# Optimization experiments

Hardware: AMD Instinct MI355X
Metric: run time of the kernel (lower is better)

## Reference

```python
import jax, jax.numpy as jnp
import numpy as np

EMBED_DIM = 1024
NUM_HEADS = 16
HEAD_DIM = EMBED_DIM // NUM_HEADS
B, T = 2, 2048


def setup_inputs() -> dict:
    key = jax.random.key(0)
    ks = jax.random.split(key, 9)
    s = 1.0 / np.sqrt(EMBED_DIM)
    return {
        "x": jax.random.normal(ks[0], (B, T, EMBED_DIM), dtype=jnp.float32),
        "W_q": jax.random.uniform(ks[1], (EMBED_DIM, EMBED_DIM), jnp.float32, -s, s),
        "b_q": jax.random.uniform(ks[2], (EMBED_DIM,), jnp.float32, -s, s),
        "W_k": jax.random.uniform(ks[3], (EMBED_DIM, EMBED_DIM), jnp.float32, -s, s),
        "b_k": jax.random.uniform(ks[4], (EMBED_DIM,), jnp.float32, -s, s),
        "W_v": jax.random.uniform(ks[5], (EMBED_DIM, EMBED_DIM), jnp.float32, -s, s),
        "b_v": jax.random.uniform(ks[6], (EMBED_DIM,), jnp.float32, -s, s),
        "W_o": jax.random.uniform(ks[7], (EMBED_DIM, EMBED_DIM), jnp.float32, -s, s),
        "b_o": jax.random.uniform(ks[8], (EMBED_DIM,), jnp.float32, -s, s),
    }


def reference(x, W_q, b_q, W_k, b_k, W_v, b_v, W_o, b_o):
    Bv, Tv, C = x.shape
    # QKV projections (torch Linear: x @ W.T + b); split into heads -> (B,H,T,Dh)
    def proj(W, b):
        return (x @ W.T + b).reshape(Bv, Tv, NUM_HEADS, HEAD_DIM).transpose(0, 2, 1, 3)
    q, k, v = proj(W_q, b_q), proj(W_k, b_k), proj(W_v, b_v)
    scale = 1.0 / np.sqrt(HEAD_DIM).astype(np.float32)
    scores = jnp.einsum("bhqd,bhkd->bhqk", q, k) * scale  # (B,H,T,T)
    causal = jnp.tril(jnp.ones((Tv, Tv), dtype=bool))
    scores = jnp.where(causal, scores, -jnp.inf)
    attn = jax.nn.softmax(scores, axis=-1)
    # dropout is identity in eval / p=0
    out = jnp.einsum("bhqk,bhkd->bhqd", attn, v)  # (B,H,T,Dh)
    out = out.transpose(0, 2, 1, 3).reshape(Bv, Tv, C)
    return out @ W_o.T + b_o
```

## Files before the change

kernel.cpp:

```cpp
#include <hip/hip_runtime.h>
#include <hip/hip_bf16.h>


typedef __bf16 bf16;
typedef __attribute__((ext_vector_type(8))) __bf16 bf16x8;
typedef __attribute__((ext_vector_type(4))) __bf16 bf16x4;
typedef __attribute__((ext_vector_type(4))) float floatx4;
typedef __attribute__((ext_vector_type(4))) short short4v;

#define LOG2E 1.44269504088896340736f

__device__ __forceinline__ void gl2lds16(const void* g, void* l) {
  __builtin_amdgcn_global_load_lds((const __attribute__((address_space(1))) void*)g,
                                   (__attribute__((address_space(3))) void*)l, 16, 0, 0);
}

__device__ __forceinline__ floatx4 mfma16(bf16x4 a, bf16x4 b, floatx4 c) {
#if __has_builtin(__builtin_amdgcn_mfma_f32_16x16x16_bf16)
  return __builtin_amdgcn_mfma_f32_16x16x16_bf16(a, b, c, 0, 0, 0);
#elif __has_builtin(__builtin_amdgcn_mfma_f32_16x16x16bf16_1k)
  return __builtin_amdgcn_mfma_f32_16x16x16bf16_1k(
      __builtin_bit_cast(short4v, a), __builtin_bit_cast(short4v, b), c, 0, 0, 0);
#else
  floatx4 d = c;
  asm volatile("v_mfma_f32_16x16x16_bf16 %0, %1, %2, %0"
               : "+v"(d) : "v"(a), "v"(b));
  return d;
#endif
}

__global__ __launch_bounds__(256) void cast_all(
    const float* __restrict__ x, const float* __restrict__ wq,
    const float* __restrict__ wk, const float* __restrict__ wv,
    const float* __restrict__ wo, bf16* __restrict__ dst)
{
  const size_t M1 = (size_t)1 << 20;
  size_t i4 = ((size_t)blockIdx.x * 256 + threadIdx.x) * 4;
  const float* src = x;
  size_t off = i4;
  if (i4 >= 4 * M1) {
    size_t r = i4 - 4 * M1;
    int seg = (int)(r >> 20);
    off = r & (M1 - 1);
    src = (seg == 0) ? wq : (seg == 1) ? wk : (seg == 2) ? wv : wo;
  }
  float4 f = *(const float4*)(src + off);
  bf16x4 o = { (bf16)f.x, (bf16)f.y, (bf16)f.z, (bf16)f.w };
  *(bf16x4*)(dst + i4) = o;
}

template<bool F32OUT, bool QKV, int BN>
__global__ __launch_bounds__(256, 3) void gemm_bt(
    const bf16* __restrict__ A, const bf16* __restrict__ Wb,
    const float* __restrict__ bq, const float* __restrict__ bk,
    const float* __restrict__ bv, void* __restrict__ outb,
    bf16* __restrict__ vt, int M, int N, int K, float qscale)
{
  __shared__ bf16 As[128 * 64];
  __shared__ bf16 Bs[BN * 64];
  const int tid = threadIdx.x;
  const int lane = tid & 63;
  const int wid = tid >> 6;
  const int l15 = lane & 15, l4 = lane >> 4;
  constexpr int I = (BN == 128) ? 4 : 2;
  const int wr = (BN == 128) ? (wid >> 1) : wid;
  const int wc = (BN == 128) ? (wid & 1) : 0;

  const bf16* W;
  const float* bias;
  float osc = 1.0f;
  int n0, mat = 0;
  bf16* outh;
  float* outf;
  if (QKV) {
    mat = blockIdx.x >> 3;
    n0 = (blockIdx.x & 7) << 7;
    W = Wb + ((size_t)mat << 20);
    bias = (mat == 0) ? bq : (mat == 1 ? bk : bv);
    if (mat == 0) osc = qscale;
    outh = (bf16*)outb + ((size_t)mat << 22);
    outf = nullptr;
  } else {
    n0 = blockIdx.x * BN;
    W = Wb;
    bias = bq;
    outf = (float*)outb;
    outh = nullptr;
  }
  const int m0 = blockIdx.y << 7;

  floatx4 acc[I][4] = {};

  for (int k0 = 0; k0 < K; k0 += 64) {
#pragma unroll
    for (int it = 0; it < 4; ++it) {
      int c = it * 256 + tid;
      int row = c >> 3, gs = ((c & 7) ^ (row & 7)) << 3;
      gl2lds16(A + (size_t)(m0 + row) * K + k0 + gs, As + c * 8);
    }
#pragma unroll
    for (int it = 0; it < BN / 32; ++it) {
      int c = it * 256 + tid;
      int row = c >> 3, gs = ((c & 7) ^ (row & 7)) << 3;
      gl2lds16(W + (size_t)(n0 + row) * K + k0 + gs, Bs + c * 8);
    }
    __syncthreads();
#pragma unroll
    for (int kk = 0; kk < 2; ++kk) {
      bf16x8 af[I], bfr[4];
#pragma unroll
      for (int i = 0; i < I; ++i) {
        int r = wr * (I * 16) + i * 16 + l15;
        int g = (kk * 4 + l4) ^ (r & 7);
        af[i] = *(const bf16x8*)(As + r * 64 + g * 8);
      }
#pragma unroll
      for (int j = 0; j < 4; ++j) {
        int r = wc * 64 + j * 16 + l15;
        int g = (kk * 4 + l4) ^ (r & 7);
        bfr[j] = *(const bf16x8*)(Bs + r * 64 + g * 8);
      }
#pragma unroll
      for (int i = 0; i < I; ++i)
#pragma unroll
        for (int j = 0; j < 4; ++j)
          acc[i][j] = __builtin_amdgcn_mfma_f32_16x16x32_bf16(af[i], bfr[j], acc[i][j], 0, 0, 0);
    }
    __syncthreads();
  }

  if (QKV && mat == 2) {
#pragma unroll
    for (int j = 0; j < 4; ++j) {
      int col = n0 + wc * 64 + j * 16 + l15;
      float bv_ = bias[col];
      int h = col >> 6, d = col & 63;
#pragma unroll
      for (int i = 0; i < I; ++i) {
        int row = m0 + wr * (I * 16) + i * 16 + l4 * 4;
        int bb = row >> 11, t = row & 2047;
        int tp = (t & ~31) | (((t >> 2) & 3) << 3) | (((t >> 4) & 1) << 2);
        bf16x4 pk;
#pragma unroll
        for (int rg = 0; rg < 4; ++rg) pk[rg] = (bf16)(acc[i][j][rg] + bv_);
        *(bf16x4*)(vt + (((size_t)(bb * 16 + h)) << 17) + ((size_t)d << 11) + tp) = pk;
      }
    }
    return;
  }

#pragma unroll
  for (int j = 0; j < 4; ++j) {
    int col = n0 + wc * 64 + j * 16 + l15;
    float bv_ = bias[col];
#pragma unroll
    for (int i = 0; i < I; ++i) {
#pragma unroll
      for (int rg = 0; rg < 4; ++rg) {
        int row = m0 + wr * (I * 16) + i * 16 + l4 * 4 + rg;
        float v = (acc[i][j][rg] + bv_) * osc;
        if (F32OUT) outf[(size_t)row * N + col] = v;
        else        outh[(size_t)row * N + col] = (bf16)v;
      }
    }
  }
}

__global__ __launch_bounds__(256, 4) void attn_kernel(
    const bf16* __restrict__ Q, const bf16* __restrict__ Kg,
    const bf16* __restrict__ Vt, bf16* __restrict__ AO)
{
  constexpr int T = 2048, C = 1024;
  __shared__ bf16 Ks[2][64 * 64];
  __shared__ bf16 Vts[2][64 * 64];

  const int tid = threadIdx.x;
  const int lane = tid & 63;
  const int w = tid >> 6;
  const int l15 = lane & 15, l4 = lane >> 4;

  const int u = blockIdx.x;
  const int bh = u & 31;
  const int qt = 31 - (u >> 5);
  const int q0 = qt << 6;
  const int nkt = qt + 1;
  const size_t base = ((size_t)(bh >> 4) * T) * C + (bh & 15) * 64;
  const bf16* vtb = Vt + ((size_t)bh << 17);

  auto stageK = [&](int j0, int bufi) {
#pragma unroll
    for (int it = 0; it < 2; ++it) {
      int c = it * 256 + tid;
      int row = c >> 3, g = (c & 7) ^ (row & 7);
      gl2lds16(Kg + base + (size_t)(j0 + row) * C + g * 8, &Ks[bufi][c * 8]);
    }
  };
  auto stageV = [&](int j0, int bufi) {
#pragma unroll
    for (int it = 0; it < 2; ++it) {
      int c = it * 256 + tid;
      int d = c >> 3, g = (c & 7) ^ (d & 7);
      gl2lds16(vtb + ((size_t)d << 11) + j0 + g * 8, &Vts[bufi][c * 8]);
    }
  };

  const int q = q0 + w * 16 + l15;

  bf16x8 qf[2];
  {
    const bf16* qp = Q + base + (size_t)q * C + l4 * 8;
    qf[0] = *(const bf16x8*)(qp);
    qf[1] = *(const bf16x8*)(qp + 32);
  }

  floatx4 o[4] = {};
  float mrow = -1e38f, lrow = 0.f;

  stageK(0, 0);
  stageV(0, 0);

  for (int jt = 0; jt < nkt; ++jt) {
    __syncthreads();
    const int cur = jt & 1;
    if (jt + 1 < nkt) {
      stageK((jt + 1) << 6, cur ^ 1);
      stageV((jt + 1) << 6, cur ^ 1);
    }
    const int j0 = jt << 6;

    floatx4 s4[4] = {};
#pragma unroll
    for (int kk = 0; kk < 2; ++kk) {
#pragma unroll
      for (int tj = 0; tj < 4; ++tj) {
        int r = tj * 16 + l15;
        int g = (kk * 4 + l4) ^ (r & 7);
        bf16x8 kf = *(const bf16x8*)(&Ks[cur][r * 64 + g * 8]);
        s4[tj] = __builtin_amdgcn_mfma_f32_16x16x32_bf16(kf, qf[kk], s4[tj], 0, 0, 0);
      }
    }

    if (jt == nkt - 1) {
#pragma unroll
      for (int tj = 0; tj < 4; ++tj) {
        int j = j0 + tj * 16 + l4 * 4;
#pragma unroll
        for (int rg = 0; rg < 4; ++rg)
          if (j + rg > q) s4[tj][rg] = -3e38f;
      }
    }

    float mx = -3e38f;
#pragma unroll
    for (int tj = 0; tj < 4; ++tj)
#pragma unroll
      for (int rg = 0; rg < 4; ++rg)
        mx = fmaxf(mx, s4[tj][rg]);
    mx = fmaxf(mx, __shfl_xor(mx, 16, 64));
    mx = fmaxf(mx, __shfl_xor(mx, 32, 64));
    float mnew = fmaxf(mrow, mx);
    float al = __builtin_amdgcn_exp2f(mrow - mnew);
    mrow = mnew;
    float ps = 0.f;
#pragma unroll
    for (int tj = 0; tj < 4; ++tj)
#pragma unroll
      for (int rg = 0; rg < 4; ++rg) {
        float e = __builtin_amdgcn_exp2f(s4[tj][rg] - mnew);
        s4[tj][rg] = e;
        ps += e;
      }
    ps += __shfl_xor(ps, 16, 64);
    ps += __shfl_xor(ps, 32, 64);
    lrow = lrow * al + ps;

    if (!__all(al == 1.f)) {
#pragma unroll
      for (int td = 0; td < 4; ++td)
#pragma unroll
        for (int rg = 0; rg < 4; ++rg)
          o[td][rg] *= al;
    }

    bf16x4 pf[4];
#pragma unroll
    for (int tj = 0; tj < 4; ++tj) {
      bf16x4 pk = { (bf16)s4[tj][0], (bf16)s4[tj][1],
                    (bf16)s4[tj][2], (bf16)s4[tj][3] };
      pf[tj] = pk;
    }

#pragma unroll
    for (int tk = 0; tk < 2; ++tk) {
#pragma unroll
      for (int td = 0; td < 4; ++td) {
        int r = td * 16 + l15;
        int g = (tk * 4 + l4) ^ (r & 7);
        bf16x8 vf = *(const bf16x8*)(&Vts[cur][r * 64 + g * 8]);
        bf16x4 lo = { vf[0], vf[1], vf[2], vf[3] };
        bf16x4 hi = { vf[4], vf[5], vf[6], vf[7] };
        o[td] = mfma16(lo, pf[tk * 2], o[td]);
        o[td] = mfma16(hi, pf[tk * 2 + 1], o[td]);
      }
    }
  }

  float inv = 1.0f / lrow;
#pragma unroll
  for (int td = 0; td < 4; ++td) {
    bf16x4 ok = { (bf16)(o[td][0] * inv), (bf16)(o[td][1] * inv),
                  (bf16)(o[td][2] * inv), (bf16)(o[td][3] * inv) };
    *(bf16x4*)(AO + base + (size_t)q * C + td * 16 + l4 * 4) = ok;
  }
}

extern "C" void kernel_launch(void* const* d_in, const int* in_sizes, int n_in,
                              void* d_out, int out_size, void* d_ws, size_t ws_size,
                              hipStream_t stream) {
  const float* x  = (const float*)d_in[0];
  const float* Wq = (const float*)d_in[1];
  const float* bq = (const float*)d_in[2];
  const float* Wk = (const float*)d_in[3];
  const float* bk = (const float*)d_in[4];
  const float* Wv = (const float*)d_in[5];
  const float* bv = (const float*)d_in[6];
  const float* Wo = (const float*)d_in[7];
  const float* bo = (const float*)d_in[8];

  bf16* ws = (bf16*)d_ws;
  const size_t M1 = (size_t)1 << 20;
  bf16* xb  = ws;
  bf16* wqb = ws + 4 * M1;
  bf16* wob = ws + 7 * M1;
  bf16* Qp  = ws + 8 * M1;
  bf16* Vtp = ws + 16 * M1;
  bf16* AOp = ws + 20 * M1;

  cast_all<<<8192, 256, 0, stream>>>(x, Wq, Wk, Wv, Wo, ws);
  gemm_bt<false, true, 128><<<dim3(24, 32), 256, 0, stream>>>(
      xb, wqb, bq, bk, bv, (void*)Qp, Vtp, 4096, 1024, 1024, 0.125f * LOG2E);
  attn_kernel<<<1024, 256, 0, stream>>>(Qp, Qp + 4 * M1, Vtp, AOp);
  gemm_bt<true, false, 64><<<dim3(16, 32), 256, 0, stream>>>(
      AOp, wob, bo, nullptr, nullptr, d_out, nullptr, 4096, 1024, 1024, 1.0f);
}
```

Measured before the change: 174.5 us.

## Fuse x cast into QKV GEMM and pair causal query tiles per attention block

Stops converting x to bf16 in a separate pass. The QKV GEMM now loads fp32 x tiles straight into LDS and converts them to bf16 when building MFMA fragments, which doubles the A-tile LDS footprint and adds conversion work inside the GEMM inner loop. Each attention block now handles two query tiles (qt and 31-qt), so every block does the same amount of causal work. The grid is halved, and K/V prefetch carries over between the two segments.

```diff
diff --git a/kernel.cpp b/kernel.cpp
--- a/kernel.cpp
+++ b/kernel.cpp
@@ -29,21 +29,16 @@
 #endif
 }
 
-__global__ __launch_bounds__(256) void cast_all(
-    const float* __restrict__ x, const float* __restrict__ wq,
-    const float* __restrict__ wk, const float* __restrict__ wv,
-    const float* __restrict__ wo, bf16* __restrict__ dst)
+__global__ __launch_bounds__(256) void cast_w(
+    const float* __restrict__ wq, const float* __restrict__ wk,
+    const float* __restrict__ wv, const float* __restrict__ wo,
+    bf16* __restrict__ dst)
 {
   const size_t M1 = (size_t)1 << 20;
   size_t i4 = ((size_t)blockIdx.x * 256 + threadIdx.x) * 4;
-  const float* src = x;
-  size_t off = i4;
-  if (i4 >= 4 * M1) {
-    size_t r = i4 - 4 * M1;
-    int seg = (int)(r >> 20);
-    off = r & (M1 - 1);
-    src = (seg == 0) ? wq : (seg == 1) ? wk : (seg == 2) ? wv : wo;
-  }
+  int seg = (int)(i4 >> 20);
+  size_t off = i4 & (M1 - 1);
+  const float* src = (seg == 0) ? wq : (seg == 1) ? wk : (seg == 2) ? wv : wo;
   float4 f = *(const float4*)(src + off);
   bf16x4 o = { (bf16)f.x, (bf16)f.y, (bf16)f.z, (bf16)f.w };
   *(bf16x4*)(dst + i4) = o;
@@ -51,12 +46,12 @@
 
 template<bool F32OUT, bool QKV, int BN>
 __global__ __launch_bounds__(256, 3) void gemm_bt(
-    const bf16* __restrict__ A, const bf16* __restrict__ Wb,
+    const void* __restrict__ Aany, const bf16* __restrict__ Wb,
     const float* __restrict__ bq, const float* __restrict__ bk,
     const float* __restrict__ bv, void* __restrict__ outb,
     bf16* __restrict__ vt, int M, int N, int K, float qscale)
 {
-  __shared__ bf16 As[128 * 64];
+  __shared__ char smemA[QKV ? 128 * 64 * 4 : 128 * 64 * 2];
   __shared__ bf16 Bs[BN * 64];
   const int tid = threadIdx.x;
   const int lane = tid & 63;
@@ -92,11 +87,25 @@
   floatx4 acc[I][4] = {};
 
   for (int k0 = 0; k0 < K; k0 += 64) {
-#pragma unroll
-    for (int it = 0; it < 4; ++it) {
-      int c = it * 256 + tid;
-      int row = c >> 3, gs = ((c & 7) ^ (row & 7)) << 3;
-      gl2lds16(A + (size_t)(m0 + row) * K + k0 + gs, As + c * 8);
+    if (QKV) {
+      const float* Af = (const float*)Aany;
+      float* Asf = (float*)smemA;
+#pragma unroll
+      for (int it = 0; it < 8; ++it) {
+        int c = it * 256 + tid;
+        int row = c >> 4, g = c & 15;
+        int gs = (g & 8) | ((g & 7) ^ (row & 7));
+        gl2lds16(Af + (size_t)(m0 + row) * K + k0 + gs * 4, Asf + c * 4);
+      }
+    } else {
+      const bf16* Ah = (const bf16*)Aany;
+      bf16* Ash = (bf16*)smemA;
+#pragma unroll
+      for (int it = 0; it < 4; ++it) {
+        int c = it * 256 + tid;
+        int row = c >> 3, gs = ((c & 7) ^ (row & 7)) << 3;
+        gl2lds16(Ah + (size_t)(m0 + row) * K + k0 + gs, Ash + c * 8);
+      }
     }
 #pragma unroll
     for (int it = 0; it < BN / 32; ++it) {
@@ -111,8 +120,21 @@
 #pragma unroll
       for (int i = 0; i < I; ++i) {
         int r = wr * (I * 16) + i * 16 + l15;
-        int g = (kk * 4 + l4) ^ (r & 7);
-        af[i] = *(const bf16x8*)(As + r * 64 + g * 8);
+        if (QKV) {
+          const float* Asf = (const float*)smemA;
+          int m2 = kk * 8 + l4 * 2;
+          int s1 = (m2 & 8) | ((m2 & 7) ^ (r & 7));
+          int s2 = ((m2 + 1) & 8) | (((m2 + 1) & 7) ^ (r & 7));
+          floatx4 fa = *(const floatx4*)(Asf + r * 64 + s1 * 4);
+          floatx4 fb = *(const floatx4*)(Asf + r * 64 + s2 * 4);
+          bf16x8 v = { (bf16)fa[0], (bf16)fa[1], (bf16)fa[2], (bf16)fa[3],
+                       (bf16)fb[0], (bf16)fb[1], (bf16)fb[2], (bf16)fb[3] };
+          af[i] = v;
+        } else {
+          const bf16* Ash = (const bf16*)smemA;
+          int g = (kk * 4 + l4) ^ (r & 7);
+          af[i] = *(const bf16x8*)(Ash + r * 64 + g * 8);
+        }
       }
 #pragma unroll
       for (int j = 0; j < 4; ++j) {
@@ -181,9 +203,7 @@
 
   const int u = blockIdx.x;
   const int bh = u & 31;
-  const int qt = 31 - (u >> 5);
-  const int q0 = qt << 6;
-  const int nkt = qt + 1;
+  const int p = u >> 5;
   const size_t base = ((size_t)(bh >> 4) * T) * C + (bh & 15) * 64;
   const bf16* vtb = Vt + ((size_t)bh << 17);
 
@@ -204,113 +224,122 @@
     }
   };
 
-  const int q = q0 + w * 16 + l15;
-
-  bf16x8 qf[2];
-  {
-    const bf16* qp = Q + base + (size_t)q * C + l4 * 8;
-    qf[0] = *(const bf16x8*)(qp);
-    qf[1] = *(const bf16x8*)(qp + 32);
-  }
-
-  floatx4 o[4] = {};
-  float mrow = -1e38f, lrow = 0.f;
-
+  const int qts[2] = { 31 - p, p };
+  int g = 0;
   stageK(0, 0);
   stageV(0, 0);
 
-  for (int jt = 0; jt < nkt; ++jt) {
-    __syncthreads();
-    const int cur = jt & 1;
-    if (jt + 1 < nkt) {
-      stageK((jt + 1) << 6, cur ^ 1);
-      stageV((jt + 1) << 6, cur ^ 1);
-    }
-    const int j0 = jt << 6;
-
-    floatx4 s4[4] = {};
-#pragma unroll
-    for (int kk = 0; kk < 2; ++kk) {
+  for (int seg = 0; seg < 2; ++seg) {
+    const int qt = qts[seg];
+    const int q0 = qt << 6;
+    const int nkt = qt + 1;
+    const int q = q0 + w * 16 + l15;
+
+    bf16x8 qf[2];
+    {
+      const bf16* qp = Q + base + (size_t)q * C + l4 * 8;
+      qf[0] = *(const bf16x8*)(qp);
+      qf[1] = *(const bf16x8*)(qp + 32);
+    }
+    floatx4 o[4] = {};
+    float mrow = -1e38f, lrow = 0.f;
+
+    for (int jt = 0; jt < nkt; ++jt, ++g) {
+      __syncthreads();
+      const int cur = g & 1;
+      if (jt + 1 < nkt) {
+        stageK((jt + 1) << 6, cur ^ 1);
+        stageV((jt + 1) << 6, cur ^ 1);
+      } else if (seg == 0) {
+        stageK(0, cur ^ 1);
+        stageV(0, cur ^ 1);
+      }
+      const int j0 = jt << 6;
+
+      floatx4 s4[4] = {};
+#pragma unroll
+      for (int kk = 0; kk < 2; ++kk) {
+#pragma unroll
+        for (int tj = 0; tj < 4; ++tj) {
+          int r = tj * 16 + l15;
+          int gg = (kk * 4 + l4) ^ (r & 7);
+          bf16x8 kf = *(const bf16x8*)(&Ks[cur][r * 64 + gg * 8]);
+          s4[tj] = __builtin_amdgcn_mfma_f32_16x16x32_bf16(kf, qf[kk], s4[tj], 0, 0, 0);
+        }
+      }
+
+      if (jt == nkt - 1) {
+#pragma unroll
+        for (int tj = 0; tj < 4; ++tj) {
+          int j = j0 + tj * 16 + l4 * 4;
+#pragma unroll
+          for (int rg = 0; rg < 4; ++rg)
+            if (j + rg > q) s4[tj][rg] = -3e38f;
+        }
+      }
+
+      float mx = -3e38f;
+#pragma unroll
+      for (int tj = 0; tj < 4; ++tj)
+#pragma unroll
+        for (int rg = 0; rg < 4; ++rg)
+          mx = fmaxf(mx, s4[tj][rg]);
+      mx = fmaxf(mx, __shfl_xor(mx, 16, 64));
+      mx = fmaxf(mx, __shfl_xor(mx, 32, 64));
+      float mnew = fmaxf(mrow, mx);
+      float al = __builtin_amdgcn_exp2f(mrow - mnew);
+      mrow = mnew;
+      float ps = 0.f;
+#pragma unroll
+      for (int tj = 0; tj < 4; ++tj)
+#pragma unroll
+        for (int rg = 0; rg < 4; ++rg) {
+          float e = __builtin_amdgcn_exp2f(s4[tj][rg] - mnew);
+          s4[tj][rg] = e;
+          ps += e;
+        }
+      ps += __shfl_xor(ps, 16, 64);
+      ps += __shfl_xor(ps, 32, 64);
+      lrow = lrow * al + ps;
+
+      if (!__all(al == 1.f)) {
+#pragma unroll
+        for (int td = 0; td < 4; ++td)
+#pragma unroll
+          for (int rg = 0; rg < 4; ++rg)
+            o[td][rg] *= al;
+      }
+
+      bf16x4 pf[4];
 #pragma unroll
       for (int tj = 0; tj < 4; ++tj) {
-        int r = tj * 16 + l15;
-        int g = (kk * 4 + l4) ^ (r & 7);
-        bf16x8 kf = *(const bf16x8*)(&Ks[cur][r * 64 + g * 8]);
-        s4[tj] = __builtin_amdgcn_mfma_f32_16x16x32_bf16(kf, qf[kk], s4[tj], 0, 0, 0);
-      }
-    }
-
-    if (jt == nkt - 1) {
-#pragma unroll
-      for (int tj = 0; tj < 4; ++tj) {
-        int j = j0 + tj * 16 + l4 * 4;
-#pragma unroll
-        for (int rg = 0; rg < 4; ++rg)
-          if (j + rg > q) s4[tj][rg] = -3e38f;
-      }
-    }
-
-    float mx = -3e38f;
-#pragma unroll
-    for (int tj = 0; tj < 4; ++tj)
-#pragma unroll
-      for (int rg = 0; rg < 4; ++rg)
-        mx = fmaxf(mx, s4[tj][rg]);
-    mx = fmaxf(mx, __shfl_xor(mx, 16, 64));
-    mx = fmaxf(mx, __shfl_xor(mx, 32, 64));
-    float mnew = fmaxf(mrow, mx);
-    float al = __builtin_amdgcn_exp2f(mrow - mnew);
-    mrow = mnew;
-    float ps = 0.f;
-#pragma unroll
-    for (int tj = 0; tj < 4; ++tj)
-#pragma unroll
-      for (int rg = 0; rg < 4; ++rg) {
-        float e = __builtin_amdgcn_exp2f(s4[tj][rg] - mnew);
-        s4[tj][rg] = e;
-        ps += e;
-      }
-    ps += __shfl_xor(ps, 16, 64);
-    ps += __shfl_xor(ps, 32, 64);
-    lrow = lrow * al + ps;
-
-    if (!__all(al == 1.f)) {
-#pragma unroll
-      for (int td = 0; td < 4; ++td)
-#pragma unroll
-        for (int rg = 0; rg < 4; ++rg)
-          o[td][rg] *= al;
-    }
-
-    bf16x4 pf[4];
-#pragma unroll
-    for (int tj = 0; tj < 4; ++tj) {
-      bf16x4 pk = { (bf16)s4[tj][0], (bf16)s4[tj][1],
-                    (bf16)s4[tj][2], (bf16)s4[tj][3] };
-      pf[tj] = pk;
-    }
-
-#pragma unroll
-    for (int tk = 0; tk < 2; ++tk) {
-#pragma unroll
-      for (int td = 0; td < 4; ++td) {
-        int r = td * 16 + l15;
-        int g = (tk * 4 + l4) ^ (r & 7);
-        bf16x8 vf = *(const bf16x8*)(&Vts[cur][r * 64 + g * 8]);
-        bf16x4 lo = { vf[0], vf[1], vf[2], vf[3] };
-        bf16x4 hi = { vf[4], vf[5], vf[6], vf[7] };
-        o[td] = mfma16(lo, pf[tk * 2], o[td]);
-        o[td] = mfma16(hi, pf[tk * 2 + 1], o[td]);
-      }
-    }
-  }
-
-  float inv = 1.0f / lrow;
-#pragma unroll
-  for (int td = 0; td < 4; ++td) {
-    bf16x4 ok = { (bf16)(o[td][0] * inv), (bf16)(o[td][1] * inv),
-                  (bf16)(o[td][2] * inv), (bf16)(o[td][3] * inv) };
-    *(bf16x4*)(AO + base + (size_t)q * C + td * 16 + l4 * 4) = ok;
+        bf16x4 pk = { (bf16)s4[tj][0], (bf16)s4[tj][1],
+                      (bf16)s4[tj][2], (bf16)s4[tj][3] };
+        pf[tj] = pk;
+      }
+
+#pragma unroll
+      for (int tk = 0; tk < 2; ++tk) {
+#pragma unroll
+        for (int td = 0; td < 4; ++td) {
+          int r = td * 16 + l15;
+          int gg = (tk * 4 + l4) ^ (r & 7);
+          bf16x8 vf = *(const bf16x8*)(&Vts[cur][r * 64 + gg * 8]);
+          bf16x4 lo = { vf[0], vf[1], vf[2], vf[3] };
+          bf16x4 hi = { vf[4], vf[5], vf[6], vf[7] };
+          o[td] = mfma16(lo, pf[tk * 2], o[td]);
+          o[td] = mfma16(hi, pf[tk * 2 + 1], o[td]);
+        }
+      }
+    }
+
+    float inv = 1.0f / lrow;
+#pragma unroll
+    for (int td = 0; td < 4; ++td) {
+      bf16x4 ok = { (bf16)(o[td][0] * inv), (bf16)(o[td][1] * inv),
+                    (bf16)(o[td][2] * inv), (bf16)(o[td][3] * inv) };
+      *(bf16x4*)(AO + base + (size_t)q * C + td * 16 + l4 * 4) = ok;
+    }
   }
 }
 
@@ -329,17 +358,18 @@
 
   bf16* ws = (bf16*)d_ws;
   const size_t M1 = (size_t)1 << 20;
-  bf16* xb  = ws;
   bf16* wqb = ws + 4 * M1;
   bf16* wob = ws + 7 * M1;
   bf16* Qp  = ws + 8 * M1;
   bf16* Vtp = ws + 16 * M1;
   bf16* AOp = ws + 20 * M1;
 
-  cast_all<<<8192, 256, 0, stream>>>(x, Wq, Wk, Wv, Wo, ws);
+  cast_w<<<4096, 256, 0, stream>>>(Wq, Wk, Wv, Wo, wqb);
   gemm_bt<false, true, 128><<<dim3(24, 32), 256, 0, stream>>>(
-      xb, wqb, bq, bk, bv, (void*)Qp, Vtp, 4096, 1024, 1024, 0.125f * LOG2E);
-  attn_kernel<<<1024, 256, 0, stream>>>(Qp, Qp + 4 * M1, Vtp, AOp);
+      (const void*)x, wqb, bq, bk, bv, (void*)Qp, Vtp, 4096, 1024, 1024,
+      0.125f * LOG2E);
+  attn_kernel<<<512, 256, 0, stream>>>(Qp, Qp + 4 * M1, Vtp, AOp);
   gemm_bt<true, false, 64><<<dim3(16, 32), 256, 0, stream>>>(
-      AOp, wob, bo, nullptr, nullptr, d_out, nullptr, 4096, 1024, 1024, 1.0f);
-}
+      (const void*)AOp, wob, bo, nullptr, nullptr, d_out, nullptr, 4096, 1024,
+      1024, 1.0f);
+}
```

New measurement: 186.7 us. 7.0% more time.
